# Optimization experiments

Measured on AMD Instinct MI355X. Metric: run time of the kernel, lower is better.

The kernel has to match this reference:

```python
import jax, jax.numpy as jnp
import numpy as np

B, S, D = 2, 1024, 4096
NQ, NKV, HD = 32, 8, 128
G = NQ // NKV
FFN = 10928  # ffn_size(4096, 4.0): int(4*4096)*2//3 = 10922 -> round up to mult of 8
ATTN_MULT = 0.08838834764831845
MAX_ATTN = 30.0
EPS = 1e-5
BASE = 10000.0


def setup_inputs() -> dict:
    key = jax.random.key(0)
    ks = jax.random.split(key, 13)
    def w(k, shape):
        return jax.random.normal(k, shape, jnp.float32) / np.float32(np.sqrt(shape[0]))
    return {
        "x": jax.random.normal(ks[0], (B, S, D), jnp.float32),
        "mask": jnp.tril(jnp.ones((1, 1, S, S), dtype=bool)),  # causal
        "scale_pre_attn": jax.random.uniform(ks[1], (D,), jnp.float32, 0.5, 1.5),
        "scale_post_attn": jax.random.uniform(ks[2], (D,), jnp.float32, 0.5, 1.5),
        "scale_pre_mlp": jax.random.uniform(ks[3], (D,), jnp.float32, 0.5, 1.5),
        "scale_post_mlp": jax.random.uniform(ks[4], (D,), jnp.float32, 0.5, 1.5),
        "wq": w(ks[5], (D, NQ * HD)),
        "wk": w(ks[6], (D, NKV * HD)),
        "wv": w(ks[7], (D, NKV * HD)),
        "wo": w(ks[8], (NQ * HD, D)),
        "w_gate": w(ks[9], (D, FFN)),
        "w_val": w(ks[10], (D, FFN)),
        "w_out": w(ks[11], (FFN, D)),
    }


def rms_norm(x, scale):
    ms = jnp.mean(jnp.square(x), axis=-1, keepdims=True)
    return x * jax.lax.rsqrt(ms + EPS) * scale


def rotate_half(x):
    x1, x2 = jnp.split(x, 2, axis=-1)
    return jnp.concatenate((-x2, x1), axis=-1)


def apply_rope(x):
    # x: [b, s, h, d]; offset=0 (no KV-cache step)
    s, d = x.shape[1], x.shape[3]
    inv_freq = 1.0 / (BASE ** (jnp.arange(0, d, 2, dtype=jnp.float32) / d))
    t = jnp.arange(s, dtype=jnp.float32)
    phase = t[:, None] * inv_freq[None, :]            # [s, d/2]
    phase = jnp.tile(phase, (1, 2))[None, :, None, :]  # [1, s, 1, d]
    return (x * jnp.cos(phase) + rotate_half(x) * jnp.sin(phase)).astype(x.dtype)


def reference(x, mask, scale_pre_attn, scale_post_attn, scale_pre_mlp, scale_post_mlp,
              wq, wk, wv, wo, w_gate, w_val, w_out):
    h = x
    # ---- attention sublayer (pre-norm) ----
    hn = rms_norm(h, scale_pre_attn)
    q = (hn @ wq).reshape(B, S, NQ, HD)
    k = (hn @ wk).reshape(B, S, NKV, HD)
    v = (hn @ wv).reshape(B, S, NKV, HD)
    q = apply_rope(q)
    k = apply_rope(k)
    qg = q.reshape(B, S, NKV, G, HD)  # GQA: group q heads per kv head
    logits = jnp.einsum("btkgd,bskd->bkgts", qg, k).astype(jnp.float32) * ATTN_MULT
    logits = MAX_ATTN * jnp.tanh(logits / MAX_ATTN)   # grok soft cap
    logits = jnp.where(mask[:, :, None], logits, -1e30)
    probs = jax.nn.softmax(logits, axis=-1).astype(x.dtype)
    attn = jnp.einsum("bkgts,bskd->btkgd", probs, v).reshape(B, S, NQ * HD)
    h_attn = attn @ wo
    h = h + rms_norm(h_attn, scale_post_attn)
    # ---- gated MLP sublayer (pre-norm) ----
    hn2 = rms_norm(h, scale_pre_mlp)
    h_dense = (jax.nn.gelu(hn2 @ w_gate) * (hn2 @ w_val)) @ w_out
    h = h + rms_norm(h_dense, scale_post_mlp)
    return h
```

## Files before the change

### kernel.cpp

```cpp
#include <hip/hip_runtime.h>
#include <stdint.h>

typedef unsigned short ushort_t;
typedef __bf16 bf16x8 __attribute__((ext_vector_type(8)));
typedef float f32x4 __attribute__((ext_vector_type(4)));

#define D_MODEL 4096
#define SEQ 1024
#define BROWS 2048
#define QKV_N 6144
#define HD 128
#define FFN_GRID 11008
#define ATTN_MULT 0.08838834764831845f

__device__ __forceinline__ unsigned short f2bf(float f){
  union { float f; unsigned u; } c; c.f = f;
  unsigned u = c.u + 0x7fffu + ((c.u >> 16) & 1u);
  return (unsigned short)(u >> 16);
}
__device__ __forceinline__ float bf2f(unsigned short h){
  union { unsigned u; float f; } c; c.u = ((unsigned)h) << 16;
  return c.f;
}
__device__ __forceinline__ f32x4 zero4(){ f32x4 z; z[0]=0.f; z[1]=0.f; z[2]=0.f; z[3]=0.f; return z; }
__device__ __forceinline__ bf16x8 ldb8(const void* p){ return *(const bf16x8*)p; }
__device__ __forceinline__ f32x4 MFMA(bf16x8 a, bf16x8 b, f32x4 c){
  return __builtin_amdgcn_mfma_f32_16x16x32_bf16(a, b, c, 0, 0, 0);
}
__device__ __forceinline__ void g2lds16(void* lds, const void* g){
  __builtin_amdgcn_global_load_lds(
      (const __attribute__((address_space(1))) void*)(uintptr_t)(g),
      (__attribute__((address_space(3))) void*)(uint32_t)(uintptr_t)(lds),
      16, 0, 0);
}
#define BAR() __builtin_amdgcn_s_barrier()
#define VMCNT8() asm volatile("s_waitcnt vmcnt(8)" ::: "memory")
#define VMCNT0() asm volatile("s_waitcnt vmcnt(0)" ::: "memory")
#define LGKM0() asm volatile("s_waitcnt lgkmcnt(0)" ::: "memory")

__global__ __launch_bounds__(256) void rmsnorm_in(const float* __restrict__ x,
                                                  const float* __restrict__ sc,
                                                  ushort_t* __restrict__ out){
  int row = blockIdx.x, tid = threadIdx.x;
  const float4* xr = (const float4*)(x + (size_t)row*D_MODEL);
  float4 v[4]; float ss = 0.f;
#pragma unroll
  for (int i=0;i<4;i++){
    v[i] = xr[tid + i*256];
    ss += v[i].x*v[i].x + v[i].y*v[i].y + v[i].z*v[i].z + v[i].w*v[i].w;
  }
#pragma unroll
  for (int m=32;m;m>>=1) ss += __shfl_xor(ss, m);
  __shared__ float red[4];
  if ((tid&63)==0) red[tid>>6] = ss;
  __syncthreads();
  float inv = rsqrtf((red[0]+red[1]+red[2]+red[3])*(1.f/4096.f) + 1e-5f);
  const float4* scv = (const float4*)sc;
#pragma unroll
  for (int i=0;i<4;i++){
    float4 s4 = scv[tid + i*256];
    ushort4 o;
    o.x = f2bf(v[i].x*inv*s4.x); o.y = f2bf(v[i].y*inv*s4.y);
    o.z = f2bf(v[i].z*inv*s4.z); o.w = f2bf(v[i].w*inv*s4.w);
    ((ushort4*)out)[(size_t)row*1024 + tid + i*256] = o;
  }
}

__global__ __launch_bounds__(256) void rmsnorm_resid(const float* __restrict__ base,
                                                     const float* __restrict__ delta,
                                                     const float* __restrict__ delta2,
                                                     const float* __restrict__ sc1,
                                                     float* __restrict__ hout,
                                                     const float* __restrict__ sc2,
                                                     ushort_t* __restrict__ hn2){
  int row = blockIdx.x, tid = threadIdx.x;
  const float4* dr = (const float4*)(delta + (size_t)row*D_MODEL);
  const float4* d2 = delta2 ? (const float4*)(delta2 + (size_t)row*D_MODEL) : nullptr;
  const float4* br = (const float4*)(base  + (size_t)row*D_MODEL);
  float4 d[4]; float ss = 0.f;
#pragma unroll
  for (int i=0;i<4;i++){
    float4 a = dr[tid + i*256];
    if (d2){
      float4 b = d2[tid + i*256];
      a.x += b.x; a.y += b.y; a.z += b.z; a.w += b.w;
    }
    d[i] = a;
    ss += d[i].x*d[i].x + d[i].y*d[i].y + d[i].z*d[i].z + d[i].w*d[i].w;
  }
#pragma unroll
  for (int m=32;m;m>>=1) ss += __shfl_xor(ss, m);
  __shared__ float red[4];
  if ((tid&63)==0) red[tid>>6] = ss;
  __syncthreads();
  float inv1 = rsqrtf((red[0]+red[1]+red[2]+red[3])*(1.f/4096.f) + 1e-5f);
  const float4* s1v = (const float4*)sc1;
  float4* ho = (float4*)(hout + (size_t)row*D_MODEL);
  float4 h4[4]; float ss2 = 0.f;
#pragma unroll
  for (int i=0;i<4;i++){
    float4 b4 = br[tid + i*256];
    float4 s4 = s1v[tid + i*256];
    float4 h;
    h.x = b4.x + d[i].x*inv1*s4.x;
    h.y = b4.y + d[i].y*inv1*s4.y;
    h.z = b4.z + d[i].z*inv1*s4.z;
    h.w = b4.w + d[i].w*inv1*s4.w;
    h4[i] = h;
    ho[tid + i*256] = h;
    ss2 += h.x*h.x + h.y*h.y + h.z*h.z + h.w*h.w;
  }
  if (sc2){
#pragma unroll
    for (int m=32;m;m>>=1) ss2 += __shfl_xor(ss2, m);
    __syncthreads();
    if ((tid&63)==0) red[tid>>6] = ss2;
    __syncthreads();
    float inv2 = rsqrtf((red[0]+red[1]+red[2]+red[3])*(1.f/4096.f) + 1e-5f);
    const float4* s2v = (const float4*)sc2;
#pragma unroll
    for (int i=0;i<4;i++){
      float4 s4 = s2v[tid + i*256];
      ushort4 o;
      o.x = f2bf(h4[i].x*inv2*s4.x); o.y = f2bf(h4[i].y*inv2*s4.y);
      o.z = f2bf(h4[i].z*inv2*s4.z); o.w = f2bf(h4[i].w*inv2*s4.w);
      ((ushort4*)hn2)[(size_t)row*1024 + tid + i*256] = o;
    }
  }
}

__global__ __launch_bounds__(256) void convT(const float* __restrict__ W,
                                             ushort_t* __restrict__ WT,
                                             int K, int N, int Kp, int Np){
  __shared__ float tile[64][65];
  int n0 = blockIdx.x*64, k0 = blockIdx.y*64;
  int tx = threadIdx.x & 63, ty = threadIdx.x >> 6;
#pragma unroll
  for (int i=0;i<16;i++){
    int k = k0 + ty + i*4, n = n0 + tx;
    tile[ty+i*4][tx] = (k < K && n < N) ? W[(size_t)k*N + n] : 0.f;
  }
  __syncthreads();
  int wtx = threadIdx.x & 15, wty = threadIdx.x >> 4;
#pragma unroll
  for (int j=0;j<4;j++){
    int n = n0 + wty + j*16;
    if (n < Np){
      ushort4 o;
      o.x = f2bf(tile[wtx*4+0][wty + j*16]);
      o.y = f2bf(tile[wtx*4+1][wty + j*16]);
      o.z = f2bf(tile[wtx*4+2][wty + j*16]);
      o.w = f2bf(tile[wtx*4+3][wty + j*16]);
      *(ushort4*)&WT[(size_t)n*Kp + k0 + wtx*4] = o;
    }
  }
}

template<int MODE, int KS>
__global__ __launch_bounds__(512, 2) void gemmW(const ushort_t* __restrict__ A, int lda,
                                                const ushort_t* __restrict__ WT, int ldw,
                                                void* __restrict__ Cv, void* __restrict__ Cv2,
                                                int ldc, int Nvalid, int K){
  __shared__ __align__(16) char smem[131072];
  const int nwg = gridDim.x;
  const int lid = blockIdx.x;
  int t = (lid & 7) * (nwg >> 3) + (lid >> 3);
  void* Cout = Cv;
  if (KS == 2){
    const int per = nwg >> 1;
    if (t >= per){ t -= per; A += (size_t)K; WT += (size_t)K; Cout = Cv2; }
  }
  const int m0 = (t & 7) << 8;
  const int n0 = (t >> 3) << 8;
  const int tid = threadIdx.x;
  const int w = tid >> 6, lane = tid & 63;
  const int wm = w >> 1, wn = w & 1;
  const int lo = lane & 15, hi = lane >> 4;
  const int srow = lane >> 3, scol = lane & 7;
  const int sw = scol ^ srow;
  const int rsw = lo & 7;
  const int NT = K >> 6;

  const ushort_t* pA = A  + (size_t)(m0 + w*8 + srow) * lda + sw*8;
  const ushort_t* pB = WT + (size_t)(n0 + w*8 + srow) * ldw + sw*8;

  auto stage = [&](int tt, int c){
    const ushort_t* g = (c < 4 ? pA + (size_t)(c*64)*lda : pB + (size_t)((c-4)*64)*ldw) + (size_t)tt*64;
    g2lds16(smem + ((tt&1)<<16) + (c < 4 ? c*8192 : 32768 + (c-4)*8192) + (w<<10), g);
  };

  f32x4 acc[4][8];
#pragma unroll
  for (int i=0;i<4;i++)
#pragma unroll
    for (int j=0;j<8;j++) acc[i][j] = zero4();

#pragma unroll
  for (int c=0;c<8;c++) stage(0, c);
#pragma unroll
  for (int c=0;c<8;c++) stage(1, c);

  for (int i=0;i<NT;i++){
    if (i == NT-1) VMCNT0(); else VMCNT8();
    BAR();
    const char* sA = smem + ((i&1)<<16);
    const char* sB = sA + 32768;
    bf16x8 af[4][2], bfr[8][2];
#pragma unroll
    for (int rf=0;rf<4;rf++)
#pragma unroll
      for (int kc=0;kc<2;kc++)
        af[rf][kc] = ldb8(sA + (wm*64 + rf*16 + lo)*128 + (((kc*4+hi)^rsw)<<4));
#pragma unroll
    for (int cf=0;cf<8;cf++)
#pragma unroll
      for (int kc=0;kc<2;kc++)
        bfr[cf][kc] = ldb8(sB + (wn*128 + cf*16 + lo)*128 + (((kc*4+hi)^rsw)<<4));
    LGKM0();
    BAR();
    if (i+2 < NT){
#pragma unroll
      for (int c=0;c<8;c++) stage(i+2, c);
    }
#pragma unroll
    for (int rf=0;rf<4;rf++)
#pragma unroll
      for (int cf=0;cf<8;cf++)
#pragma unroll
        for (int kc=0;kc<2;kc++)
          acc[rf][cf] = MFMA(af[rf][kc], bfr[cf][kc], acc[rf][cf]);
  }
#pragma unroll
  for (int rf=0;rf<4;rf++){
#pragma unroll
    for (int cf=0;cf<8;cf++){
#pragma unroll
      for (int r=0;r<4;r++){
        int m = m0 + wm*64 + rf*16 + hi*4 + r;
        int n = n0 + wn*128 + cf*16 + lo;
        if (n < Nvalid){
          float v = acc[rf][cf][r];
          size_t idx = (size_t)m*ldc + n;
          if (MODE == 1) ((float*)Cout)[idx] = v;
          else           ((ushort_t*)Cout)[idx] = f2bf(v);
        }
      }
    }
  }
}

__global__ __launch_bounds__(512, 2) void gemm_gv(const ushort_t* __restrict__ A, int lda,
                                                  const ushort_t* __restrict__ B1,
                                                  const ushort_t* __restrict__ B2, int ldw,
                                                  ushort_t* __restrict__ Cv, int ldc,
                                                  int Nvalid, int K){
  __shared__ __align__(16) char smem[131072];
  const int nwg = gridDim.x;
  const int lid = blockIdx.x;
  const int t  = (lid & 7) * (nwg >> 3) + (lid >> 3);
  const int m0 = (t & 7) << 8;
  const int n0 = (t >> 3) << 7;
  const int tid = threadIdx.x;
  const int w = tid >> 6, lane = tid & 63;
  const int wm = w >> 1, wn = w & 1;
  const int lo = lane & 15, hi = lane >> 4;
  const int srow = lane >> 3, scol = lane & 7;
  const int sw = scol ^ srow;
  const int rsw = lo & 7;
  const int NT = K >> 6;

  const ushort_t* pA  = A  + (size_t)(m0 + w*8 + srow) * lda + sw*8;
  const ushort_t* pB1 = B1 + (size_t)(n0 + w*8 + srow) * ldw + sw*8;
  const ushort_t* pB2 = B2 + (size_t)(n0 + w*8 + srow) * ldw + sw*8;

  auto stage = [&](int tt, int c){
    const ushort_t* g;
    int lofs;
    if (c < 4){ g = pA  + (size_t)(c*64)*lda;     lofs = c*8192; }
    else if (c < 6){ g = pB1 + (size_t)((c-4)*64)*ldw; lofs = 32768 + (c-4)*8192; }
    else { g = pB2 + (size_t)((c-6)*64)*ldw; lofs = 49152 + (c-6)*8192; }
    g2lds16(smem + ((tt&1)<<16) + lofs + (w<<10), g + (size_t)tt*64);
  };

  f32x4 ag[4][4], av[4][4];
#pragma unroll
  for (int i=0;i<4;i++)
#pragma unroll
    for (int j=0;j<4;j++){ ag[i][j] = zero4(); av[i][j] = zero4(); }

#pragma unroll
  for (int c=0;c<8;c++) stage(0, c);
#pragma unroll
  for (int c=0;c<8;c++) stage(1, c);

  for (int i=0;i<NT;i++){
    if (i == NT-1) VMCNT0(); else VMCNT8();
    BAR();
    const char* sA  = smem + ((i&1)<<16);
    const char* sB1 = sA + 32768;
    const char* sB2 = sA + 49152;
    bf16x8 af[4][2], b1f[4][2], b2f[4][2];
#pragma unroll
    for (int rf=0;rf<4;rf++)
#pragma unroll
      for (int kc=0;kc<2;kc++)
        af[rf][kc] = ldb8(sA + (wm*64 + rf*16 + lo)*128 + (((kc*4+hi)^rsw)<<4));
#pragma unroll
    for (int cf=0;cf<4;cf++)
#pragma unroll
      for (int kc=0;kc<2;kc++){
        b1f[cf][kc] = ldb8(sB1 + (wn*64 + cf*16 + lo)*128 + (((kc*4+hi)^rsw)<<4));
        b2f[cf][kc] = ldb8(sB2 + (wn*64 + cf*16 + lo)*128 + (((kc*4+hi)^rsw)<<4));
      }
    LGKM0();
    BAR();
    if (i+2 < NT){
#pragma unroll
      for (int c=0;c<8;c++) stage(i+2, c);
    }
#pragma unroll
    for (int rf=0;rf<4;rf++)
#pragma unroll
      for (int cf=0;cf<4;cf++)
#pragma unroll
        for (int kc=0;kc<2;kc++){
          ag[rf][cf] = MFMA(af[rf][kc], b1f[cf][kc], ag[rf][cf]);
          av[rf][cf] = MFMA(af[rf][kc], b2f[cf][kc], av[rf][cf]);
        }
  }
#pragma unroll
  for (int rf=0;rf<4;rf++){
#pragma unroll
    for (int cf=0;cf<4;cf++){
#pragma unroll
      for (int r=0;r<4;r++){
        int m = m0 + wm*64 + rf*16 + hi*4 + r;
        int n = n0 + wn*64 + cf*16 + lo;
        if (n < Nvalid){
          float g = ag[rf][cf][r];
          float v = av[rf][cf][r];
          float ga = 0.5f*g*(1.f + tanhf(0.7978845608028654f*(g + 0.044715f*g*g*g)));
          Cv[(size_t)m*ldc + n] = f2bf(ga * v);
        }
      }
    }
  }
}

__global__ void rope_tab_kernel(float* __restrict__ tab){
  int s = blockIdx.x, i = threadIdx.x;
  float invf = __expf(-(float)i * (9.210340371976184f/64.f));
  float ph = (float)s * invf;
  float sn, cs;
  sincosf(ph, &sn, &cs);
  tab[s*128 + i] = cs;
  tab[s*128 + 64 + i] = sn;
}

__global__ __launch_bounds__(256) void rope_apply(ushort_t* __restrict__ qkv,
                                                  const float* __restrict__ tab){
  int idx = blockIdx.x*256 + threadIdx.x;
  int pr = idx & 63;
  int h  = (idx >> 6) % 40;
  int row = idx / 2560;
  int t = row & (SEQ-1);
  ushort_t* p = qkv + (size_t)row*QKV_N + h*HD + pr;
  float c = tab[t*128 + pr], s = tab[t*128 + 64 + pr];
  float x1 = bf2f(p[0]), x2 = bf2f(p[64]);
  p[0]  = f2bf(x1*c - x2*s);
  p[64] = f2bf(x2*c + x1*s);
}

__global__ __launch_bounds__(256) void transpose_v(const ushort_t* __restrict__ qkv,
                                                   ushort_t* __restrict__ VT){
  __shared__ ushort_t tile[32][33];
  int d0 = blockIdx.x*32, m0 = blockIdx.y*32;
  int tx = threadIdx.x & 31, ty = threadIdx.x >> 5;
#pragma unroll
  for (int i=0;i<4;i++)
    tile[ty + i*8][tx] = qkv[(size_t)(m0 + ty + i*8)*QKV_N + 5120 + d0 + tx];
  __syncthreads();
#pragma unroll
  for (int i=0;i<4;i++)
    VT[(size_t)(d0 + ty + i*8)*BROWS + m0 + tx] = tile[tx][ty + i*8];
}

__global__ __launch_bounds__(256) void attn_kernel(const ushort_t* __restrict__ qkv,
                                                   const ushort_t* __restrict__ VT,
                                                   ushort_t* __restrict__ outp){
  const int blk = blockIdx.x;
  const int bh = blk & 63;
  const int tgrp = 15 - (blk >> 6);
  const int b = bh >> 5, qh = bh & 31, kv = qh >> 2;
  const int w = threadIdx.x >> 6, lane = threadIdx.x & 63;
  const int lo = lane & 15, hi = lane >> 4;
  const int t0 = tgrp*64 + w*16;
  __shared__ ushort_t P[4][16][72];
  ushort_t (*Pw)[72] = P[w];

  const ushort_t* Qb = qkv + (size_t)(b*SEQ + t0 + lo)*QKV_N + qh*HD + hi*8;
  bf16x8 qf[4];
#pragma unroll
  for (int c=0;c<4;c++) qf[c] = ldb8(Qb + c*32);

  f32x4 of[8];
#pragma unroll
  for (int i=0;i<8;i++) of[i] = zero4();
  float ls[4] = {0.f,0.f,0.f,0.f};

  const ushort_t* Kb = qkv + (size_t)(b*SEQ + lo)*QKV_N + D_MODEL + kv*HD + hi*8;
  const ushort_t* Vb = VT + (size_t)(kv*HD + lo)*BROWS + b*SEQ + hi*8;

  const int nst = tgrp + 1;
  for (int st=0; st<nst; st++){
    const int s0 = st*64;
    f32x4 sacc[4];
#pragma unroll
    for (int nf=0;nf<4;nf++) sacc[nf] = zero4();
#pragma unroll
    for (int c=0;c<4;c++){
#pragma unroll
      for (int nf=0;nf<4;nf++){
        bf16x8 kf = ldb8(Kb + (size_t)(s0 + nf*16)*QKV_N + c*32);
        sacc[nf] = MFMA(qf[c], kf, sacc[nf]);
      }
    }
#pragma unroll
    for (int nf=0;nf<4;nf++){
#pragma unroll
      for (int r=0;r<4;r++){
        int tq = t0 + hi*4 + r;
        int s = s0 + nf*16 + lo;
        float xx = sacc[nf][r] * ATTN_MULT;
        float z = fminf(fmaxf(xx*(2.f/30.f), -80.f), 80.f);
        float e = __expf(z);
        float th = (e - 1.f)/(e + 1.f);
        float p = (s <= tq) ? __expf(30.f*th - 30.f) : 0.f;
        ls[r] += p;
        Pw[hi*4+r][nf*16+lo] = f2bf(p);
      }
    }
    __builtin_amdgcn_sched_barrier(0);
    __builtin_amdgcn_s_waitcnt(0xc07f);
    __builtin_amdgcn_sched_barrier(0);
#pragma unroll
    for (int c2=0;c2<2;c2++){
      bf16x8 pf = ldb8(&Pw[lo][c2*32 + hi*8]);
#pragma unroll
      for (int nf2=0;nf2<8;nf2++){
        bf16x8 vf = ldb8(Vb + (size_t)(nf2*16)*BROWS + s0 + c2*32);
        of[nf2] = MFMA(pf, vf, of[nf2]);
      }
    }
    __builtin_amdgcn_sched_barrier(0);
  }
#pragma unroll
  for (int m=1;m<16;m<<=1){
#pragma unroll
    for (int r=0;r<4;r++) ls[r] += __shfl_xor(ls[r], m);
  }
  float inv[4];
#pragma unroll
  for (int r=0;r<4;r++) inv[r] = 1.f/ls[r];
  ushort_t* Ob = outp + (size_t)(b*SEQ + t0 + hi*4)*D_MODEL + qh*HD + lo;
#pragma unroll
  for (int nf2=0;nf2<8;nf2++)
#pragma unroll
    for (int r=0;r<4;r++)
      Ob[(size_t)r*D_MODEL + nf2*16] = f2bf(of[nf2][r]*inv[r]);
}

extern "C" void kernel_launch(void* const* d_in, const int* in_sizes, int n_in,
                              void* d_out, int out_size, void* d_ws, size_t ws_size,
                              hipStream_t stream){
  const float* x        = (const float*)d_in[0];
  const float* sc_pre_a = (const float*)d_in[2];
  const float* sc_post_a= (const float*)d_in[3];
  const float* sc_pre_m = (const float*)d_in[4];
  const float* sc_post_m= (const float*)d_in[5];
  const float* wq  = (const float*)d_in[6];
  const float* wk  = (const float*)d_in[7];
  const float* wv  = (const float*)d_in[8];
  const float* wo  = (const float*)d_in[9];
  const float* wg  = (const float*)d_in[10];
  const float* wva = (const float*)d_in[11];
  const float* wou = (const float*)d_in[12];

  char* ws = (char*)d_ws;
  size_t off = 0;
  auto alloc = [&](size_t bytes)->void*{
    void* p = ws + off; off += (bytes + 255) & ~(size_t)255; return p;
  };
  ushort_t* WT   = (ushort_t*)alloc((size_t)FFN_GRID*D_MODEL*2);
  ushort_t* hn   = (ushort_t*)alloc((size_t)BROWS*D_MODEL*2);
  ushort_t* qkv  = (ushort_t*)alloc((size_t)BROWS*QKV_N*2);
  ushort_t* VT   = (ushort_t*)alloc((size_t)SEQ*BROWS*2);
  ushort_t* attn = (ushort_t*)alloc((size_t)BROWS*D_MODEL*2);
  float*    tmp32= (float*)alloc((size_t)BROWS*D_MODEL*4);
  ushort_t* hn2  = (ushort_t*)alloc((size_t)BROWS*D_MODEL*2);
  ushort_t* act  = (ushort_t*)alloc((size_t)BROWS*FFN_GRID*2);
  float*    rtab = (float*)alloc((size_t)SEQ*128*4);
  float* h = (float*)d_out;
  ushort_t* WT2  = (ushort_t*)hn;
  float* part_o  = (float*)act;
  float* part_u  = (float*)hn;

  rmsnorm_in<<<BROWS, 256, 0, stream>>>(x, sc_pre_a, hn);
  convT<<<dim3(64, 64), 256, 0, stream>>>(wq, WT,                     4096, 4096, 4096, 4096);
  convT<<<dim3(16, 64), 256, 0, stream>>>(wk, WT + (size_t)4096*4096, 4096, 1024, 4096, 1024);
  convT<<<dim3(16, 64), 256, 0, stream>>>(wv, WT + (size_t)5120*4096, 4096, 1024, 4096, 1024);
  gemmW<0,1><<<192, 512, 0, stream>>>(hn, 4096, WT, 4096, qkv, nullptr, QKV_N, QKV_N, 4096);
  rope_tab_kernel<<<SEQ, 64, 0, stream>>>(rtab);
  rope_apply<<<(BROWS*40*64)/256, 256, 0, stream>>>(qkv, rtab);
  transpose_v<<<dim3(32,64), 256, 0, stream>>>(qkv, VT);
  attn_kernel<<<1024, 256, 0, stream>>>(qkv, VT, attn);
  convT<<<dim3(64, 64), 256, 0, stream>>>(wo, WT, 4096, 4096, 4096, 4096);
  gemmW<1,2><<<256, 512, 0, stream>>>(attn, 4096, WT, 4096, tmp32, part_o, 4096, 4096, 2048);
  rmsnorm_resid<<<BROWS, 256, 0, stream>>>(x, tmp32, part_o, sc_post_a, h, sc_pre_m, hn2);
  convT<<<dim3(172, 64), 256, 0, stream>>>(wg,  WT,  4096, 10928, 4096, FFN_GRID);
  convT<<<dim3(172, 64), 256, 0, stream>>>(wva, WT2, 4096, 10928, 4096, FFN_GRID);
  gemm_gv<<<688, 512, 0, stream>>>(hn2, 4096, WT, WT2, 4096, act, FFN_GRID, FFN_GRID, 4096);
  convT<<<dim3(64, 172), 256, 0, stream>>>(wou, WT, 10928, 4096, FFN_GRID, 4096);
  gemmW<1,2><<<256, 512, 0, stream>>>(act, FFN_GRID, WT, FFN_GRID, tmp32, part_u, 4096, 4096, 5504);
  rmsnorm_resid<<<BROWS, 256, 0, stream>>>(h, tmp32, part_u, sc_post_m, h, nullptr, nullptr);
}
```

Measured before the change: 1.202 ms.

## Interleave LDS fragment loads with MFMAs and vectorize weight transpose-convert

In both GEMM kernels, the explicit lgkmcnt(0) wait before the barrier is removed and the MFMA loop now sits before the barrier and the next-stage prefetch. A sched_barrier stops the compiler from moving work across that point. This lets LDS reads overlap with matrix-core work instead of draining before compute, but the global prefetch for tile i+2 now issues later, after the compute. Separately, the weight transpose/convert kernel now uses float4 global loads and 16-byte bf16 stores, with a padded LDS tile.

Measured after the change: 1.162 ms. 1.03x faster.

```diff
diff --git a/kernel.cpp b/kernel.cpp
--- a/kernel.cpp
+++ b/kernel.cpp
@@ -2,6 +2,7 @@
 #include <stdint.h>
 
 typedef unsigned short ushort_t;
+typedef unsigned short us8 __attribute__((ext_vector_type(8)));
 typedef __bf16 bf16x8 __attribute__((ext_vector_type(8)));
 typedef float f32x4 __attribute__((ext_vector_type(4)));
 
@@ -36,7 +37,7 @@
 #define BAR() __builtin_amdgcn_s_barrier()
 #define VMCNT8() asm volatile("s_waitcnt vmcnt(8)" ::: "memory")
 #define VMCNT0() asm volatile("s_waitcnt vmcnt(0)" ::: "memory")
-#define LGKM0() asm volatile("s_waitcnt lgkmcnt(0)" ::: "memory")
+#define SGB0() __builtin_amdgcn_sched_barrier(0)
 
 __global__ __launch_bounds__(256) void rmsnorm_in(const float* __restrict__ x,
                                                   const float* __restrict__ sc,
@@ -132,26 +133,36 @@
 __global__ __launch_bounds__(256) void convT(const float* __restrict__ W,
                                              ushort_t* __restrict__ WT,
                                              int K, int N, int Kp, int Np){
-  __shared__ float tile[64][65];
+  __shared__ float tile[64][69];
+  int tx = threadIdx.x & 15, ty = threadIdx.x >> 4;
   int n0 = blockIdx.x*64, k0 = blockIdx.y*64;
-  int tx = threadIdx.x & 63, ty = threadIdx.x >> 6;
-#pragma unroll
-  for (int i=0;i<16;i++){
-    int k = k0 + ty + i*4, n = n0 + tx;
-    tile[ty+i*4][tx] = (k < K && n < N) ? W[(size_t)k*N + n] : 0.f;
+#pragma unroll
+  for (int i=0;i<4;i++){
+    int k = k0 + ty + i*16, n = n0 + tx*4;
+    float4 v;
+    if (k < K && n + 3 < N){
+      v = *(const float4*)&W[(size_t)k*N + n];
+    } else {
+      v.x = (k<K && n+0<N) ? W[(size_t)k*N + n+0] : 0.f;
+      v.y = (k<K && n+1<N) ? W[(size_t)k*N + n+1] : 0.f;
+      v.z = (k<K && n+2<N) ? W[(size_t)k*N + n+2] : 0.f;
+      v.w = (k<K && n+3<N) ? W[(size_t)k*N + n+3] : 0.f;
+    }
+    tile[ty+i*16][tx*4+0] = v.x;
+    tile[ty+i*16][tx*4+1] = v.y;
+    tile[ty+i*16][tx*4+2] = v.z;
+    tile[ty+i*16][tx*4+3] = v.w;
   }
   __syncthreads();
-  int wtx = threadIdx.x & 15, wty = threadIdx.x >> 4;
-#pragma unroll
-  for (int j=0;j<4;j++){
-    int n = n0 + wty + j*16;
+  int kc = (threadIdx.x & 7)*8, nr = threadIdx.x >> 3;
+#pragma unroll
+  for (int j=0;j<2;j++){
+    int n = n0 + nr + j*32;
     if (n < Np){
-      ushort4 o;
-      o.x = f2bf(tile[wtx*4+0][wty + j*16]);
-      o.y = f2bf(tile[wtx*4+1][wty + j*16]);
-      o.z = f2bf(tile[wtx*4+2][wty + j*16]);
-      o.w = f2bf(tile[wtx*4+3][wty + j*16]);
-      *(ushort4*)&WT[(size_t)n*Kp + k0 + wtx*4] = o;
+      us8 o;
+#pragma unroll
+      for (int i=0;i<8;i++) o[i] = f2bf(tile[kc+i][nr + j*32]);
+      *(us8*)&WT[(size_t)n*Kp + k0 + kc] = o;
     }
   }
 }
@@ -216,19 +227,19 @@
 #pragma unroll
       for (int kc=0;kc<2;kc++)
         bfr[cf][kc] = ldb8(sB + (wn*128 + cf*16 + lo)*128 + (((kc*4+hi)^rsw)<<4));
-    LGKM0();
+#pragma unroll
+    for (int rf=0;rf<4;rf++)
+#pragma unroll
+      for (int cf=0;cf<8;cf++)
+#pragma unroll
+        for (int kc=0;kc<2;kc++)
+          acc[rf][cf] = MFMA(af[rf][kc], bfr[cf][kc], acc[rf][cf]);
+    SGB0();
     BAR();
     if (i+2 < NT){
 #pragma unroll
       for (int c=0;c<8;c++) stage(i+2, c);
     }
-#pragma unroll
-    for (int rf=0;rf<4;rf++)
-#pragma unroll
-      for (int cf=0;cf<8;cf++)
-#pragma unroll
-        for (int kc=0;kc<2;kc++)
-          acc[rf][cf] = MFMA(af[rf][kc], bfr[cf][kc], acc[rf][cf]);
   }
 #pragma unroll
   for (int rf=0;rf<4;rf++){
@@ -312,12 +323,6 @@
         b1f[cf][kc] = ldb8(sB1 + (wn*64 + cf*16 + lo)*128 + (((kc*4+hi)^rsw)<<4));
         b2f[cf][kc] = ldb8(sB2 + (wn*64 + cf*16 + lo)*128 + (((kc*4+hi)^rsw)<<4));
       }
-    LGKM0();
-    BAR();
-    if (i+2 < NT){
-#pragma unroll
-      for (int c=0;c<8;c++) stage(i+2, c);
-    }
 #pragma unroll
     for (int rf=0;rf<4;rf++)
 #pragma unroll
@@ -327,6 +332,12 @@
           ag[rf][cf] = MFMA(af[rf][kc], b1f[cf][kc], ag[rf][cf]);
           av[rf][cf] = MFMA(af[rf][kc], b2f[cf][kc], av[rf][cf]);
         }
+    SGB0();
+    BAR();
+    if (i+2 < NT){
+#pragma unroll
+      for (int c=0;c<8;c++) stage(i+2, c);
+    }
   }
 #pragma unroll
   for (int rf=0;rf<4;rf++){
```
